# Optimization experiments

Measured on AMD Instinct MI355X. Metric: run time of the kernel, lower is better.

## Reference

```python
import jax, jax.numpy as jnp
import numpy as np
import math

IN_C = 512
OUT_C = 512
K = 3
STYLE = 512
EPS = 1e-8
MOD_SCALE = 1.0 / math.sqrt(STYLE)        # EqualLinear scale (lr_mul=1)
CONV_SCALE = 1.0 / math.sqrt(IN_C * K * K)  # ModulatedConv2d scale


def setup_inputs() -> dict:
    key = jax.random.key(0)
    k1, k2, k3, k4 = jax.random.split(key, 4)
    return {
        "x": jax.random.normal(k1, (8, IN_C, 64, 64), dtype=jnp.float32),
        "style": jax.random.normal(k2, (8, STYLE), dtype=jnp.float32),
        "mod_weight": jax.random.normal(k3, (IN_C, STYLE), dtype=jnp.float32),
        "mod_bias": jnp.ones((IN_C,), dtype=jnp.float32),
        "weight": jax.random.normal(k4, (1, OUT_C, IN_C, K, K), dtype=jnp.float32),
    }


def _per_sample_conv(xi, wi):
    # xi: [in_c, H, W], wi: [out_c, in_c, K, K]
    out = jax.lax.conv_general_dilated(
        xi[None], wi, window_strides=(1, 1), padding="SAME",
        dimension_numbers=("NCHW", "OIHW", "NCHW"))
    return out[0]


def reference(x, style, mod_weight, mod_bias, weight):
    # EqualLinear modulation: s = style @ (W*scale)^T + bias  -> [B, in_c]
    s = style @ (mod_weight * MOD_SCALE).T + mod_bias
    # per-sample modulated weight: [B, out_c, in_c, K, K]
    w = CONV_SCALE * weight * s[:, None, :, None, None]
    demod = jax.lax.rsqrt(jnp.sum(w * w, axis=(2, 3, 4), keepdims=True) + EPS)
    w = w * demod
    # grouped conv (groups=batch) == vmap of per-sample conv
    out = jax.vmap(_per_sample_conv)(x, w)  # [B, out_c, H, W]
    return out
```

## Files before the change

kernel.cpp:

```cpp
#include <hip/hip_runtime.h>
#include <hip/hip_bf16.h>

typedef __attribute__((ext_vector_type(8))) short bf16x8;
typedef __attribute__((ext_vector_type(4))) float f32x4;
typedef unsigned int u32;

#define MOD_SCALE 0.04419417382415922f
#define CONV_SCALE 0.014731391274719742f

__device__ __forceinline__ unsigned short f2bf(float f) {
  union { float f; u32 u; } v; v.f = f;
  u32 r = v.u + 0x7fffu + ((v.u >> 16) & 1u);
  return (unsigned short)(r >> 16);
}

__device__ __forceinline__ void gload_lds16(const void* g, void* l) {
  __builtin_amdgcn_global_load_lds(
      (const __attribute__((address_space(1))) u32*)g,
      (__attribute__((address_space(3))) u32*)l, 16, 0, 0);
}

__global__ void k_style(const float* __restrict__ style, const float* __restrict__ mw,
                        const float* __restrict__ mb, float* __restrict__ s) {
  int idx = blockIdx.x * 256 + threadIdx.x;
  int b = idx >> 9, ic = idx & 511;
  const float4* wr = (const float4*)(mw + ic * 512);
  const float4* sr = (const float4*)(style + b * 512);
  float acc = 0.f;
  #pragma unroll 4
  for (int k = 0; k < 128; ++k) {
    float4 a = wr[k], c = sr[k];
    acc += a.x * c.x + a.y * c.y + a.z * c.z + a.w * c.w;
  }
  s[idx] = acc * MOD_SCALE + mb[ic];
}

__global__ void k_wprep(const float* __restrict__ wsrc, ushort* __restrict__ wb,
                        float* __restrict__ wsq, float* __restrict__ zerobuf) {
  int idx = blockIdx.x * 256 + threadIdx.x;
  if (blockIdx.x == 0 && threadIdx.x < 16) zerobuf[threadIdx.x] = 0.f;
  const float* wp = wsrc + (size_t)idx * 9;
  float sq = 0.f;
  #pragma unroll
  for (int tap = 0; tap < 9; ++tap) {
    float v = wp[tap];
    sq += v * v;
    wb[tap * 262144 + idx] = f2bf(v);
  }
  wsq[idx] = sq;
}

__global__ void k_demod(const float* __restrict__ wsq, const float* __restrict__ s,
                        float* __restrict__ dscale) {
  int idx = blockIdx.x * 256 + threadIdx.x;
  int b = idx >> 9, oc = idx & 511;
  const float4* wq = (const float4*)(wsq + oc * 512);
  const float4* sp = (const float4*)(s + b * 512);
  float acc = 0.f;
  #pragma unroll 4
  for (int k = 0; k < 128; ++k) {
    float4 a = wq[k], c = sp[k];
    acc += a.x * c.x * c.x + a.y * c.y * c.y + a.z * c.z * c.z + a.w * c.w * c.w;
  }
  dscale[idx] = CONV_SCALE * rsqrtf(CONV_SCALE * CONV_SCALE * acc + 1e-8f);
}

__global__ void k_xform(const float* __restrict__ x, const float* __restrict__ s,
                        ushort* __restrict__ xsb) {
  const int y = blockIdx.x, b = blockIdx.y, ich = blockIdx.z;
  const int t = threadIdx.x;
  __shared__ ushort T[64 * 264];
  const int px = t & 63, iq = t >> 6;
  const int icbase = ich * 256;
  #pragma unroll
  for (int i = 0; i < 8; ++i) {
    int ic8 = i * 4 + iq;
    int ic0 = icbase + ic8 * 8;
    union { ushort u[8]; uint4 v; } pk;
    #pragma unroll
    for (int j = 0; j < 8; ++j) {
      int ic = ic0 + j;
      float v = x[(b * 512 + ic) * 4096 + y * 64 + px] * s[b * 512 + ic];
      pk.u[j] = f2bf(v);
    }
    *(uint4*)&T[px * 264 + ic8 * 8] = pk.v;
  }
  __syncthreads();
  const int ch = t & 31;
  ushort* obase = xsb + ((b * 64 + y) * 64) * 512 + icbase + ch * 8;
  #pragma unroll
  for (int i = 0; i < 8; ++i) {
    int p = i * 8 + (t >> 5);
    uint4 v = *(const uint4*)&T[p * 264 + ch * 8];
    *(uint4*)(obase + p * 512) = v;
  }
}

#define BUFB 79104
__global__ __launch_bounds__(512, 1) void k_conv(
    const ushort* __restrict__ wb, const ushort* __restrict__ xsb,
    const float* __restrict__ dscale, const float* __restrict__ zerobuf,
    float* __restrict__ out) {
  const int yb = blockIdx.x, ocb = blockIdx.y, b = blockIdx.z;
  const int t = threadIdx.x;
  const int wv = t >> 6, l = t & 63;
  const int ln = l & 15, lq = l >> 4;
  const int y0 = yb * 8;

  extern __shared__ char smem[];
  float* dss = (float*)(smem + 2 * BUFB);

  if (t < 64) dss[t] = dscale[b * 512 + ocb * 64 + t];

  f32x4 acc[4][4];
  #pragma unroll
  for (int m = 0; m < 4; ++m)
    #pragma unroll
    for (int n = 0; n < 4; ++n)
      acc[m][n] = f32x4{0.f, 0.f, 0.f, 0.f};

  const int aslot = lq ^ ((ln >> 1) & 3);
  int bslot[3];
  #pragma unroll
  for (int dx = 0; dx < 3; ++dx) bslot[dx] = lq ^ (((ln + dx) >> 1) & 3);

  const int a_ocl = (t & 255) >> 2;
  const int a_qs = (t & 3) ^ ((a_ocl >> 1) & 3);
  const int a_tb = t >> 8;
  const char* srcA = (const char*)(wb + (ocb * 64 + a_ocl) * 512 + a_qs * 8);
  const int a_dstw = wv * 1024;

  int bpart[6];
  const char* bsrc[6];
  int bdstc[6];
  #pragma unroll
  for (int i = 0; i < 6; ++i) {
    int cid = i * 512 + t;
    int r = cid / 264;
    int rem = cid - r * 264;
    int c = rem >> 2, q = rem & 3;
    int yy = y0 - 1 + r, xx = c - 1;
    int qs = q ^ ((c >> 1) & 3);
    bpart[i] = (cid < 2640);
    int geo_ok = bpart[i] && ((unsigned)yy < 64u) && ((unsigned)xx < 64u);
    bsrc[i] = geo_ok ? (const char*)(xsb + ((b * 64 + yy) * 64 + xx) * 512 + qs * 8)
                     : (const char*)nullptr;
    bdstc[i] = (i * 512 + wv * 64) * 16;
  }

  auto STAGE = [&](int boff, int icB) {
    char* Ab = smem + boff;
    char* Bb = smem + boff + 36864;
    #pragma unroll
    for (int i = 0; i < 4; ++i) {
      int tap = 2 * i + a_tb;
      gload_lds16(srcA + tap * 524288 + icB, Ab + i * 8192 + a_dstw);
    }
    if (t < 256)
      gload_lds16(srcA + 8 * 524288 + icB, Ab + 4 * 8192 + a_dstw);
    #pragma unroll
    for (int i = 0; i < 6; ++i) {
      if (bpart[i]) {
        const char* src = bsrc[i] ? bsrc[i] + icB : (const char*)zerobuf;
        gload_lds16(src, Bb + bdstc[i]);
      }
    }
  };

  auto COMPUTE = [&](int boff) {
    const char* Ab = smem + boff;
    const char* Bb = smem + boff + 36864;
    #pragma unroll
    for (int dy = 0; dy < 3; ++dy) {
      const int row = wv + dy;
      #pragma unroll
      for (int dx = 0; dx < 3; ++dx) {
        const int tap = dy * 3 + dx;
        bf16x8 af[4], bfr[4];
        #pragma unroll
        for (int m = 0; m < 4; ++m)
          af[m] = *(const bf16x8*)(Ab + tap * 4096 + (m * 16 + ln) * 64 + aslot * 16);
        #pragma unroll
        for (int n = 0; n < 4; ++n)
          bfr[n] = *(const bf16x8*)(Bb + (row * 66 + n * 16 + ln + dx) * 64 + bslot[dx] * 16);
        #pragma unroll
        for (int m = 0; m < 4; ++m)
          #pragma unroll
          for (int n = 0; n < 4; ++n)
            acc[m][n] = __builtin_amdgcn_mfma_f32_16x16x32_bf16(af[m], bfr[n], acc[m][n], 0, 0, 0);
      }
    }
  };

  STAGE(0, 0);
  __syncthreads();
  #pragma unroll 1
  for (int it = 0; it < 16; ++it) {
    if (it < 15) STAGE(((it + 1) & 1) * BUFB, (it + 1) * 64);
    COMPUTE((it & 1) * BUFB);
    __syncthreads();
  }

  const int y_row = y0 + wv;
  #pragma unroll
  for (int m = 0; m < 4; ++m) {
    #pragma unroll
    for (int r4 = 0; r4 < 4; ++r4) {
      const int oc_l = m * 16 + lq * 4 + r4;
      const float sc = dss[oc_l];
      float* op = out + ((b * 512 + ocb * 64 + oc_l) * 4096 + y_row * 64);
      #pragma unroll
      for (int n = 0; n < 4; ++n)
        op[n * 16 + ln] = acc[m][n][r4] * sc;
    }
  }
}

extern "C" void kernel_launch(void* const* d_in, const int* in_sizes, int n_in,
                              void* d_out, int out_size, void* d_ws, size_t ws_size,
                              hipStream_t stream) {
  const float* x     = (const float*)d_in[0];
  const float* style = (const float*)d_in[1];
  const float* mw    = (const float*)d_in[2];
  const float* mb    = (const float*)d_in[3];
  const float* wsrc  = (const float*)d_in[4];
  float* out = (float*)d_out;

  char* ws = (char*)d_ws;
  float*  zerobuf = (float*)(ws + 0);
  float*  s       = (float*)(ws + 256);
  float*  dscale  = (float*)(ws + 16640);
  float*  wsq     = (float*)(ws + 33024);
  ushort* wb      = (ushort*)(ws + 1081600);
  ushort* xsb     = (ushort*)(ws + 5800192);

  hipFuncSetAttribute(reinterpret_cast<const void*>(k_conv),
                      hipFuncAttributeMaxDynamicSharedMemorySize, 2 * BUFB + 256);

  k_style<<<dim3(16), dim3(256), 0, stream>>>(style, mw, mb, s);
  k_wprep<<<dim3(1024), dim3(256), 0, stream>>>(wsrc, wb, wsq, zerobuf);
  k_demod<<<dim3(16), dim3(256), 0, stream>>>(wsq, s, dscale);
  k_xform<<<dim3(64, 8, 2), dim3(256), 0, stream>>>(x, s, xsb);
  k_conv<<<dim3(8, 8, 8), dim3(512), 2 * BUFB + 256, stream>>>(wb, xsb, dscale, zerobuf, out);
}
```

Before: 190.2 us.

## Compute two output rows per wave in conv and merge style/weight prep kernels

The conv block drops from 8 to 4 waves (512 to 256 threads), and each wave now computes two output rows. Each B fragment loaded from LDS is reused across the dy taps, which cuts LDS read traffic per MFMA. The staging loops are rewritten for 256 threads. The style GEMV and weight-prep kernels are fused into one launch to save a kernel launch. The trade-off is doubled accumulator registers and fewer waves per CU to hide latency.

Result: no change. 187.2 us (-1.6%).

```diff
diff --git a/kernel.cpp b/kernel.cpp
--- a/kernel.cpp
+++ b/kernel.cpp
@@ -20,34 +20,35 @@
       (__attribute__((address_space(3))) u32*)l, 16, 0, 0);
 }
 
-__global__ void k_style(const float* __restrict__ style, const float* __restrict__ mw,
-                        const float* __restrict__ mb, float* __restrict__ s) {
-  int idx = blockIdx.x * 256 + threadIdx.x;
-  int b = idx >> 9, ic = idx & 511;
-  const float4* wr = (const float4*)(mw + ic * 512);
-  const float4* sr = (const float4*)(style + b * 512);
-  float acc = 0.f;
-  #pragma unroll 4
-  for (int k = 0; k < 128; ++k) {
-    float4 a = wr[k], c = sr[k];
-    acc += a.x * c.x + a.y * c.y + a.z * c.z + a.w * c.w;
-  }
-  s[idx] = acc * MOD_SCALE + mb[ic];
-}
-
-__global__ void k_wprep(const float* __restrict__ wsrc, ushort* __restrict__ wb,
-                        float* __restrict__ wsq, float* __restrict__ zerobuf) {
-  int idx = blockIdx.x * 256 + threadIdx.x;
-  if (blockIdx.x == 0 && threadIdx.x < 16) zerobuf[threadIdx.x] = 0.f;
-  const float* wp = wsrc + (size_t)idx * 9;
-  float sq = 0.f;
-  #pragma unroll
-  for (int tap = 0; tap < 9; ++tap) {
-    float v = wp[tap];
-    sq += v * v;
-    wb[tap * 262144 + idx] = f2bf(v);
-  }
-  wsq[idx] = sq;
+__global__ void k_prep(const float* __restrict__ wsrc, ushort* __restrict__ wb,
+                       float* __restrict__ wsq, float* __restrict__ zerobuf,
+                       const float* __restrict__ style, const float* __restrict__ mw,
+                       const float* __restrict__ mb, float* __restrict__ s) {
+  if (blockIdx.x < 1024) {
+    int idx = blockIdx.x * 256 + threadIdx.x;
+    if (blockIdx.x == 0 && threadIdx.x < 16) zerobuf[threadIdx.x] = 0.f;
+    const float* wp = wsrc + (size_t)idx * 9;
+    float sq = 0.f;
+    #pragma unroll
+    for (int tap = 0; tap < 9; ++tap) {
+      float v = wp[tap];
+      sq += v * v;
+      wb[tap * 262144 + idx] = f2bf(v);
+    }
+    wsq[idx] = sq;
+  } else {
+    int idx = (blockIdx.x - 1024) * 256 + threadIdx.x;
+    int b = idx >> 9, ic = idx & 511;
+    const float4* wr = (const float4*)(mw + ic * 512);
+    const float4* sr = (const float4*)(style + b * 512);
+    float acc = 0.f;
+    #pragma unroll 4
+    for (int k = 0; k < 128; ++k) {
+      float4 a = wr[k], c = sr[k];
+      acc += a.x * c.x + a.y * c.y + a.z * c.z + a.w * c.w;
+    }
+    s[idx] = acc * MOD_SCALE + mb[ic];
+  }
 }
 
 __global__ void k_demod(const float* __restrict__ wsq, const float* __restrict__ s,
@@ -97,7 +98,7 @@
 }
 
 #define BUFB 79104
-__global__ __launch_bounds__(512, 1) void k_conv(
+__global__ __launch_bounds__(256, 1) void k_conv(
     const ushort* __restrict__ wb, const ushort* __restrict__ xsb,
     const float* __restrict__ dscale, const float* __restrict__ zerobuf,
     float* __restrict__ out) {
@@ -112,58 +113,55 @@
 
   if (t < 64) dss[t] = dscale[b * 512 + ocb * 64 + t];
 
-  f32x4 acc[4][4];
-  #pragma unroll
-  for (int m = 0; m < 4; ++m)
-    #pragma unroll
-    for (int n = 0; n < 4; ++n)
-      acc[m][n] = f32x4{0.f, 0.f, 0.f, 0.f};
+  f32x4 acc[2][4][4];
+  #pragma unroll
+  for (int rr = 0; rr < 2; ++rr)
+    #pragma unroll
+    for (int m = 0; m < 4; ++m)
+      #pragma unroll
+      for (int n = 0; n < 4; ++n)
+        acc[rr][m][n] = f32x4{0.f, 0.f, 0.f, 0.f};
 
   const int aslot = lq ^ ((ln >> 1) & 3);
   int bslot[3];
   #pragma unroll
   for (int dx = 0; dx < 3; ++dx) bslot[dx] = lq ^ (((ln + dx) >> 1) & 3);
 
-  const int a_ocl = (t & 255) >> 2;
+  const int a_ocl = t >> 2;
   const int a_qs = (t & 3) ^ ((a_ocl >> 1) & 3);
-  const int a_tb = t >> 8;
   const char* srcA = (const char*)(wb + (ocb * 64 + a_ocl) * 512 + a_qs * 8);
   const int a_dstw = wv * 1024;
 
-  int bpart[6];
-  const char* bsrc[6];
-  int bdstc[6];
-  #pragma unroll
-  for (int i = 0; i < 6; ++i) {
-    int cid = i * 512 + t;
+  const char* bsrc[11];
+  int bdstc[11];
+  #pragma unroll
+  for (int i = 0; i < 11; ++i) {
+    int cid = i * 256 + t;
     int r = cid / 264;
     int rem = cid - r * 264;
     int c = rem >> 2, q = rem & 3;
     int yy = y0 - 1 + r, xx = c - 1;
     int qs = q ^ ((c >> 1) & 3);
-    bpart[i] = (cid < 2640);
-    int geo_ok = bpart[i] && ((unsigned)yy < 64u) && ((unsigned)xx < 64u);
+    int geo_ok = (cid < 2640) && ((unsigned)yy < 64u) && ((unsigned)xx < 64u);
     bsrc[i] = geo_ok ? (const char*)(xsb + ((b * 64 + yy) * 64 + xx) * 512 + qs * 8)
                      : (const char*)nullptr;
-    bdstc[i] = (i * 512 + wv * 64) * 16;
+    bdstc[i] = (i * 256 + wv * 64) * 16;
   }
 
   auto STAGE = [&](int boff, int icB) {
     char* Ab = smem + boff;
     char* Bb = smem + boff + 36864;
     #pragma unroll
-    for (int i = 0; i < 4; ++i) {
-      int tap = 2 * i + a_tb;
-      gload_lds16(srcA + tap * 524288 + icB, Ab + i * 8192 + a_dstw);
-    }
-    if (t < 256)
-      gload_lds16(srcA + 8 * 524288 + icB, Ab + 4 * 8192 + a_dstw);
-    #pragma unroll
-    for (int i = 0; i < 6; ++i) {
-      if (bpart[i]) {
-        const char* src = bsrc[i] ? bsrc[i] + icB : (const char*)zerobuf;
-        gload_lds16(src, Bb + bdstc[i]);
-      }
+    for (int i = 0; i < 9; ++i)
+      gload_lds16(srcA + i * 524288 + icB, Ab + i * 4096 + a_dstw);
+    #pragma unroll
+    for (int i = 0; i < 10; ++i) {
+      const char* src = bsrc[i] ? bsrc[i] + icB : (const char*)zerobuf;
+      gload_lds16(src, Bb + bdstc[i]);
+    }
+    if (t < 80) {
+      const char* src = bsrc[10] ? bsrc[10] + icB : (const char*)zerobuf;
+      gload_lds16(src, Bb + bdstc[10]);
     }
   };
 
@@ -171,23 +169,27 @@
     const char* Ab = smem + boff;
     const char* Bb = smem + boff + 36864;
     #pragma unroll
-    for (int dy = 0; dy < 3; ++dy) {
-      const int row = wv + dy;
-      #pragma unroll
-      for (int dx = 0; dx < 3; ++dx) {
+    for (int dx = 0; dx < 3; ++dx) {
+      bf16x8 bfr[4][4];
+      #pragma unroll
+      for (int r4 = 0; r4 < 4; ++r4)
+        #pragma unroll
+        for (int n = 0; n < 4; ++n)
+          bfr[r4][n] = *(const bf16x8*)(Bb + ((wv * 2 + r4) * 66 + n * 16 + ln + dx) * 64 + bslot[dx] * 16);
+      #pragma unroll
+      for (int dy = 0; dy < 3; ++dy) {
         const int tap = dy * 3 + dx;
-        bf16x8 af[4], bfr[4];
+        bf16x8 af[4];
         #pragma unroll
         for (int m = 0; m < 4; ++m)
           af[m] = *(const bf16x8*)(Ab + tap * 4096 + (m * 16 + ln) * 64 + aslot * 16);
         #pragma unroll
-        for (int n = 0; n < 4; ++n)
-          bfr[n] = *(const bf16x8*)(Bb + (row * 66 + n * 16 + ln + dx) * 64 + bslot[dx] * 16);
-        #pragma unroll
-        for (int m = 0; m < 4; ++m)
+        for (int rr = 0; rr < 2; ++rr)
           #pragma unroll
-          for (int n = 0; n < 4; ++n)
-            acc[m][n] = __builtin_amdgcn_mfma_f32_16x16x32_bf16(af[m], bfr[n], acc[m][n], 0, 0, 0);
+          for (int m = 0; m < 4; ++m)
+            #pragma unroll
+            for (int n = 0; n < 4; ++n)
+              acc[rr][m][n] = __builtin_amdgcn_mfma_f32_16x16x32_bf16(af[m], bfr[dy + rr][n], acc[rr][m][n], 0, 0, 0);
       }
     }
   };
@@ -201,17 +203,20 @@
     __syncthreads();
   }
 
-  const int y_row = y0 + wv;
-  #pragma unroll
-  for (int m = 0; m < 4; ++m) {
-    #pragma unroll
-    for (int r4 = 0; r4 < 4; ++r4) {
-      const int oc_l = m * 16 + lq * 4 + r4;
-      const float sc = dss[oc_l];
-      float* op = out + ((b * 512 + ocb * 64 + oc_l) * 4096 + y_row * 64);
-      #pragma unroll
-      for (int n = 0; n < 4; ++n)
-        op[n * 16 + ln] = acc[m][n][r4] * sc;
+  #pragma unroll
+  for (int rr = 0; rr < 2; ++rr) {
+    const int y_row = y0 + wv * 2 + rr;
+    #pragma unroll
+    for (int m = 0; m < 4; ++m) {
+      #pragma unroll
+      for (int r4 = 0; r4 < 4; ++r4) {
+        const int oc_l = m * 16 + lq * 4 + r4;
+        const float sc = dss[oc_l];
+        float* op = out + ((b * 512 + ocb * 64 + oc_l) * 4096 + y_row * 64);
+        #pragma unroll
+        for (int n = 0; n < 4; ++n)
+          op[n * 16 + ln] = acc[rr][m][n][r4] * sc;
+      }
     }
   }
 }
@@ -237,9 +242,8 @@
   hipFuncSetAttribute(reinterpret_cast<const void*>(k_conv),
                       hipFuncAttributeMaxDynamicSharedMemorySize, 2 * BUFB + 256);
 
-  k_style<<<dim3(16), dim3(256), 0, stream>>>(style, mw, mb, s);
-  k_wprep<<<dim3(1024), dim3(256), 0, stream>>>(wsrc, wb, wsq, zerobuf);
+  k_prep<<<dim3(1040), dim3(256), 0, stream>>>(wsrc, wb, wsq, zerobuf, style, mw, mb, s);
   k_demod<<<dim3(16), dim3(256), 0, stream>>>(wsq, s, dscale);
   k_xform<<<dim3(64, 8, 2), dim3(256), 0, stream>>>(x, s, xsb);
-  k_conv<<<dim3(8, 8, 8), dim3(512), 2 * BUFB + 256, stream>>>(wb, xsb, dscale, zerobuf, out);
-}
+  k_conv<<<dim3(8, 8, 8), dim3(256), 2 * BUFB + 256, stream>>>(wb, xsb, dscale, zerobuf, out);
+}
```
